# Kernel optimization log

Hardware: AMD Instinct MI355X
Metric: run time of the kernel (lower is better)

## Reference

```python
import jax, jax.numpy as jnp
import numpy as np

B, S, D = 4, 2048, 1024
H, DK, DV = 16, 64, 64


def setup_inputs() -> dict:
    key = jax.random.key(0)
    ks = jax.random.split(key, 12)
    sd = 1.0 / np.sqrt(D)
    sdo = 1.0 / np.sqrt(DV * H)
    return {
        "query": jax.random.normal(ks[0], (B, S, D), jnp.float32),
        "key": jax.random.normal(ks[1], (B, S, D), jnp.float32),
        "value": jax.random.normal(ks[2], (B, S, D), jnp.float32),
        "mask": jnp.zeros((B, 1, 1, S), jnp.float32),
        "Wq": jax.random.uniform(ks[3], (D, DK * H), jnp.float32, -sd, sd),
        "bq": jax.random.uniform(ks[4], (DK * H,), jnp.float32, -sd, sd),
        "Wk": jax.random.uniform(ks[5], (D, DK * H), jnp.float32, -sd, sd),
        "bk": jax.random.uniform(ks[6], (DK * H,), jnp.float32, -sd, sd),
        "Wv": jax.random.uniform(ks[7], (D, DV * H), jnp.float32, -sd, sd),
        "bv": jax.random.uniform(ks[8], (DV * H,), jnp.float32, -sd, sd),
        "Wo": jax.random.uniform(ks[9], (DV * H, D), jnp.float32, -sdo, sdo),
        "bo": jax.random.uniform(ks[10], (D,), jnp.float32, -sdo, sdo),
    }


def reference(query, key, value, mask, Wq, bq, Wk, bk, Wv, bv, Wo, bo):
    b, sq, _ = query.shape
    # QKV projections -> (B, H, S, d)
    Q = (query @ Wq + bq).reshape(b, sq, H, DK).transpose(0, 2, 1, 3)
    K = (key @ Wk + bk).reshape(b, key.shape[1], H, DK).transpose(0, 2, 1, 3)
    V = (value @ Wv + bv).reshape(b, value.shape[1], H, DV).transpose(0, 2, 1, 3)
    # scaled dot-product attention with additive mask
    scores = jnp.einsum("bhqd,bhkd->bhqk", Q, K) / jnp.sqrt(jnp.float32(DK))
    scores = scores + mask  # mask broadcast over heads/query positions
    probs = jax.nn.softmax(scores, axis=-1)
    # weighted values, merge heads -> (B, S, H*DV)
    weights = jnp.einsum("bhqk,bhkd->bhqd", probs, V).transpose(0, 2, 1, 3).reshape(b, sq, H * DV)
    output = weights @ Wo + bo  # dropout p=0 (eval) -> identity
    return (output, weights)
```

## Files before the change

kernel.cpp:

```cpp
#include <hip/hip_runtime.h>
#include <hip/hip_bf16.h>

typedef __attribute__((ext_vector_type(8))) short bf16x8;
typedef __attribute__((ext_vector_type(8))) short short8v;
typedef __attribute__((ext_vector_type(4))) float f32x4;

__device__ __forceinline__ short f2bf(float x) {
  union { __hip_bfloat16 h; short s; } u;
  u.h = __float2bfloat16(x);
  return u.s;
}

__device__ __forceinline__ void async16(const void* g, void* l) {
  __builtin_amdgcn_global_load_lds(
      (const __attribute__((address_space(1))) unsigned int*)g,
      (__attribute__((address_space(3))) unsigned int*)l, 16, 0, 0);
}

#define VM_WAIT4 do { asm volatile("s_waitcnt vmcnt(4)" ::: "memory"); \
                      __builtin_amdgcn_sched_barrier(0); } while (0)
#define VM_WAIT0 do { asm volatile("s_waitcnt vmcnt(0)" ::: "memory"); \
                      __builtin_amdgcn_sched_barrier(0); } while (0)

__device__ __forceinline__ void stage8k(const char* gbase, int rowStride, short* lds, int tid) {
  int wave = tid >> 6, lane = tid & 63;
#pragma unroll
  for (int j = 0; j < 2; ++j) {
    int chunk = wave * 128 + j * 64 + lane;
    int row = chunk >> 3;
    int colb = (chunk & 7) << 4;
    const char* src = gbase + row * rowStride + (colb ^ ((row & 7) << 4));
    char* dst = (char*)lds + (wave * 128 + j * 64) * 16;
    async16(src, dst);
  }
}

__global__ __launch_bounds__(256) void cvtw_k(const float* Wq, const float* Wk,
                                              const float* Wv, const float* Wo, short* Wt) {
  __shared__ short T[64 * 72];
  int mat = blockIdx.z;
  const float* src = mat == 0 ? Wq : (mat == 1 ? Wk : (mat == 2 ? Wv : Wo));
  int n0 = blockIdx.x * 64, k0 = blockIdx.y * 64;
  int tid = threadIdx.x;
#pragma unroll
  for (int i = 0; i < 4; ++i) {
    int f = i * 256 + tid;
    int kk = f >> 4, nn4 = (f & 15) * 4;
    float4 v = *(const float4*)(src + (size_t)(k0 + kk) * 1024 + n0 + nn4);
    short* d = &T[kk * 72 + nn4];
    d[0] = f2bf(v.x); d[1] = f2bf(v.y); d[2] = f2bf(v.z); d[3] = f2bf(v.w);
  }
  __syncthreads();
  short* dstm = Wt + (size_t)mat * 1048576;
#pragma unroll
  for (int i = 0; i < 2; ++i) {
    int cidx = i * 256 + tid;
    int nn = cidx >> 3, kc = (cidx & 7) * 8;
    short8v o;
#pragma unroll
    for (int j = 0; j < 8; ++j) o[j] = T[(kc + j) * 72 + nn];
    *(short8v*)(dstm + (size_t)(n0 + nn) * 1024 + k0 + kc) = o;
  }
}

__global__ __launch_bounds__(256) void cvta_k(const float* q, const float* k,
                                              const float* v, short* out) {
  int z = blockIdx.y;
  const float* src = z == 0 ? q : (z == 1 ? k : v);
  size_t base = ((size_t)blockIdx.x * 256 + threadIdx.x) * 8;
  float4 a = *(const float4*)(src + base);
  float4 b2 = *(const float4*)(src + base + 4);
  short8v h;
  h[0] = f2bf(a.x);  h[1] = f2bf(a.y);  h[2] = f2bf(a.z);  h[3] = f2bf(a.w);
  h[4] = f2bf(b2.x); h[5] = f2bf(b2.y); h[6] = f2bf(b2.z); h[7] = f2bf(b2.w);
  *(short8v*)(out + (size_t)z * 8388608 + base) = h;
}

template <int MODE>
__global__ __launch_bounds__(256) void gemm_k(
    const short* Ab, const short* Wt, const float* bias0, const float* bias1,
    short* Qp, short* Kp, short* Vpt, float* outF) {
  __shared__ short As[2][128 * 32];
  __shared__ short Bs[2][128 * 32];
  int tid = threadIdx.x, lane = tid & 63, wave = tid >> 6;
  int g = lane >> 4, c = lane & 15;
  int orig = blockIdx.x + blockIdx.y * 8;
  int wg = (orig & 7) * 64 + (orig >> 3);
  int n0 = (wg & 7) * 128, m0 = (wg >> 3) * 128, z = blockIdx.z;

  const short* Az = (MODE == 0) ? Ab + (size_t)z * 8388608 : Ab;
  const short* Wz = (MODE == 0) ? Wt + (size_t)z * 1048576 : Wt;
  const float* bias = (MODE == 0) ? (z == 0 ? bias0 : bias1) : bias0;

  auto stage = [&](int ks, int buf) {
    const char* ga = (const char*)Az + ((size_t)m0 * 1024 + ks * 32) * 2;
    const char* gb = (const char*)Wz + ((size_t)n0 * 1024 + ks * 32) * 2;
#pragma unroll
    for (int i = 0; i < 2; ++i) {
      int ch = i * 256 + tid;
      int row = ch >> 2, slot = ch & 3;
      int sw = ((row >> 1) & 3) << 4;
      char* dstA = (char*)&As[buf][0] + (i * 256 + wave * 64) * 16;
      char* dstB = (char*)&Bs[buf][0] + (i * 256 + wave * 64) * 16;
      async16(ga + (size_t)row * 2048 + ((slot << 4) ^ sw), dstA);
      async16(gb + (size_t)row * 2048 + ((slot << 4) ^ sw), dstB);
    }
  };

  f32x4 acc[4][4];
#pragma unroll
  for (int i = 0; i < 4; ++i)
#pragma unroll
    for (int j = 0; j < 4; ++j) acc[i][j] = (f32x4){0.f, 0.f, 0.f, 0.f};

  int wr = (wave >> 1) * 64, wc = (wave & 1) * 64;

  stage(0, 0);
  for (int ks = 0; ks < 32; ++ks) {
    if (ks + 1 < 32) { stage(ks + 1, (ks & 1) ^ 1); VM_WAIT4; }
    else             { VM_WAIT0; }
    __builtin_amdgcn_s_barrier();
    int cur = ks & 1;
    bf16x8 af[4], bfv[4];
#pragma unroll
    for (int mt = 0; mt < 4; ++mt) {
      int r_ = wr + mt * 16 + c;
      af[mt] = *(const bf16x8*)((const char*)&As[cur][0] + r_ * 64 +
                                ((g << 4) ^ ((((r_ >> 1) & 3)) << 4)));
    }
#pragma unroll
    for (int nt = 0; nt < 4; ++nt) {
      int r_ = wc + nt * 16 + c;
      bfv[nt] = *(const bf16x8*)((const char*)&Bs[cur][0] + r_ * 64 +
                                 ((g << 4) ^ ((((r_ >> 1) & 3)) << 4)));
    }
    __builtin_amdgcn_s_setprio(1);
#pragma unroll
    for (int mt = 0; mt < 4; ++mt)
#pragma unroll
      for (int nt = 0; nt < 4; ++nt) {
        if (MODE == 1)
          acc[mt][nt] = __builtin_amdgcn_mfma_f32_16x16x32_bf16(af[mt], bfv[nt], acc[mt][nt], 0, 0, 0);
        else
          acc[mt][nt] = __builtin_amdgcn_mfma_f32_16x16x32_bf16(bfv[nt], af[mt], acc[mt][nt], 0, 0, 0);
      }
    __builtin_amdgcn_s_setprio(0);
    __builtin_amdgcn_s_barrier();
  }

  if (MODE == 0) {
    short* dst0 = (z == 0) ? Qp : Kp;
    float scale = (z == 0) ? 0.125f : 1.f;
#pragma unroll
    for (int nt = 0; nt < 4; ++nt) {
      int nb = n0 + wc + nt * 16 + g * 4;
      float4 b4 = *(const float4*)(bias + nb);
      int d0 = nb & 63, nh = nb >> 6;
#pragma unroll
      for (int mt = 0; mt < 4; ++mt) {
        int m = m0 + wr + mt * 16 + c;
        int bh = (m >> 11) * 16 + nh;
        short4 hv;
        hv.x = f2bf((acc[mt][nt][0] + b4.x) * scale);
        hv.y = f2bf((acc[mt][nt][1] + b4.y) * scale);
        hv.z = f2bf((acc[mt][nt][2] + b4.z) * scale);
        hv.w = f2bf((acc[mt][nt][3] + b4.w) * scale);
        *(short4*)(dst0 + ((size_t)bh * 2048 + (m & 2047)) * 64 + d0) = hv;
      }
    }
  } else if (MODE == 1) {
#pragma unroll
    for (int nt = 0; nt < 4; ++nt) {
      int n = n0 + wc + nt * 16 + c;
      float bb = bias[n];
      int d = n & 63, nh = n >> 6;
#pragma unroll
      for (int mt = 0; mt < 4; ++mt) {
        int mb = m0 + wr + mt * 16 + g * 4;
        int bh = (mb >> 11) * 16 + nh;
        short4 hv;
        hv.x = f2bf(acc[mt][nt][0] + bb);
        hv.y = f2bf(acc[mt][nt][1] + bb);
        hv.z = f2bf(acc[mt][nt][2] + bb);
        hv.w = f2bf(acc[mt][nt][3] + bb);
        *(short4*)(Vpt + ((size_t)bh * 64 + d) * 2048 + (mb & 2047)) = hv;
      }
    }
  } else {
#pragma unroll
    for (int nt = 0; nt < 4; ++nt) {
      int nb = n0 + wc + nt * 16 + g * 4;
      float4 b4 = *(const float4*)(bias + nb);
#pragma unroll
      for (int mt = 0; mt < 4; ++mt) {
        int m = m0 + wr + mt * 16 + c;
        float4 o;
        o.x = acc[mt][nt][0] + b4.x;
        o.y = acc[mt][nt][1] + b4.y;
        o.z = acc[mt][nt][2] + b4.z;
        o.w = acc[mt][nt][3] + b4.w;
        *(float4*)(outF + (size_t)m * 1024 + nb) = o;
      }
    }
  }
}

__global__ __launch_bounds__(256) void attn_k(const short* Qp, const short* Kp,
                                              const short* Vpt, const float* mask,
                                              float* outW, short* wbf) {
  __shared__ short Qs[64 * 64];
  __shared__ short Ks[2][64 * 64];
  __shared__ short Vs[2][64 * 64];
  short* Ps = Qs;
  int tid = threadIdx.x, lane = tid & 63, wave = tid >> 6;
  int g = lane >> 4, c = lane & 15;
  int orig = blockIdx.x + blockIdx.y * 32;
  int wg = (orig & 7) * 256 + (orig >> 3);
  int qt = wg & 31, bh = wg >> 5;
  int b = bh >> 4, h = bh & 15;

  const char* Qg = (const char*)Qp + ((size_t)bh * 2048 + qt * 64) * 128;
  const char* Kg = (const char*)Kp + (size_t)bh * 2048 * 128;
  const char* Vg = (const char*)Vpt + (size_t)bh * 64 * 4096;

  stage8k(Qg, 128, Qs, tid);
  stage8k(Kg, 128, Ks[0], tid);
  stage8k(Vg, 4096, Vs[0], tid);

  f32x4 acco[4];
#pragma unroll
  for (int i = 0; i < 4; ++i) acco[i] = (f32x4){0.f, 0.f, 0.f, 0.f};
  float mrun = -1e30f, lrun = 0.f;

  VM_WAIT4;
  int qrow = wave * 16 + c;
  bf16x8 aq[2];
#pragma unroll
  for (int k2 = 0; k2 < 2; ++k2)
    aq[k2] = *(const bf16x8*)((const char*)Qs + qrow * 128 +
                              ((k2 * 64 + g * 16) ^ ((qrow & 7) << 4)));

  int cur = 0;
  for (int t = 0; t < 32; ++t) {
    float4 mk[4];
#pragma unroll
    for (int n = 0; n < 4; ++n)
      mk[n] = *(const float4*)(mask + (size_t)b * 2048 + t * 64 + n * 16 + g * 4);
    __builtin_amdgcn_sched_barrier(0);
    if (t + 1 < 32) {
      stage8k(Kg + (size_t)(t + 1) * 8192, 128, Ks[cur ^ 1], tid);
      stage8k(Vg + (size_t)(t + 1) * 128, 4096, Vs[cur ^ 1], tid);
    }
    VM_WAIT4;
    __builtin_amdgcn_s_barrier();
    f32x4 sc[4];
    __builtin_amdgcn_s_setprio(1);
#pragma unroll
    for (int n = 0; n < 4; ++n) {
      sc[n] = (f32x4){0.f, 0.f, 0.f, 0.f};
#pragma unroll
      for (int k2 = 0; k2 < 2; ++k2) {
        int row = n * 16 + c;
        bf16x8 bk = *(const bf16x8*)((const char*)&Ks[cur][0] + row * 128 +
                                     ((k2 * 64 + g * 16) ^ ((row & 7) << 4)));
        sc[n] = __builtin_amdgcn_mfma_f32_16x16x32_bf16(bk, aq[k2], sc[n], 0, 0, 0);
      }
    }
    __builtin_amdgcn_s_setprio(0);
#pragma unroll
    for (int n = 0; n < 4; ++n) {
      sc[n][0] += mk[n].x; sc[n][1] += mk[n].y;
      sc[n][2] += mk[n].z; sc[n][3] += mk[n].w;
    }
    float tmax = sc[0][0];
#pragma unroll
    for (int n = 0; n < 4; ++n)
#pragma unroll
      for (int r = 0; r < 4; ++r) tmax = fmaxf(tmax, sc[n][r]);
    tmax = fmaxf(tmax, __shfl_xor(tmax, 16));
    tmax = fmaxf(tmax, __shfl_xor(tmax, 32));
    if (!__all(tmax <= mrun + 8.0f)) {
      float mnew = fmaxf(mrun, tmax);
      float fsc = __expf(mrun - mnew);
      mrun = mnew;
      lrun *= fsc;
#pragma unroll
      for (int n = 0; n < 4; ++n)
#pragma unroll
        for (int r = 0; r < 4; ++r) acco[n][r] *= fsc;
    }
    float p[4][4], rs = 0.f;
#pragma unroll
    for (int n = 0; n < 4; ++n)
#pragma unroll
      for (int r = 0; r < 4; ++r) {
        p[n][r] = __expf(sc[n][r] - mrun);
        rs += p[n][r];
      }
    rs += __shfl_xor(rs, 16);
    rs += __shfl_xor(rs, 32);
    lrun += rs;
#pragma unroll
    for (int n = 0; n < 4; ++n) {
      short4 hv;
      hv.x = f2bf(p[n][0]); hv.y = f2bf(p[n][1]);
      hv.z = f2bf(p[n][2]); hv.w = f2bf(p[n][3]);
      int colb = (n * 32 + g * 8) ^ ((qrow & 7) << 4);
      *(short4*)((char*)Ps + qrow * 128 + colb) = hv;
    }
    __builtin_amdgcn_s_setprio(1);
#pragma unroll
    for (int k2 = 0; k2 < 2; ++k2) {
      bf16x8 ap = *(const bf16x8*)((const char*)Ps + qrow * 128 +
                                   ((k2 * 64 + g * 16) ^ ((qrow & 7) << 4)));
#pragma unroll
      for (int n2 = 0; n2 < 4; ++n2) {
        int rv = n2 * 16 + c;
        bf16x8 bv = *(const bf16x8*)((const char*)&Vs[cur][0] + rv * 128 +
                                     ((k2 * 64 + g * 16) ^ ((rv & 7) << 4)));
        acco[n2] = __builtin_amdgcn_mfma_f32_16x16x32_bf16(bv, ap, acco[n2], 0, 0, 0);
      }
    }
    __builtin_amdgcn_s_setprio(0);
    __builtin_amdgcn_s_barrier();
    cur ^= 1;
  }
  float inv = 1.0f / lrun;
  int srow = qt * 64 + qrow;
#pragma unroll
  for (int n = 0; n < 4; ++n) {
    int col0 = h * 64 + n * 16 + g * 4;
    size_t idx = ((size_t)b * 2048 + srow) * 1024 + col0;
    float4 o;
    o.x = acco[n][0] * inv; o.y = acco[n][1] * inv;
    o.z = acco[n][2] * inv; o.w = acco[n][3] * inv;
    *(float4*)(outW + idx) = o;
    short4 hv;
    hv.x = f2bf(o.x); hv.y = f2bf(o.y); hv.z = f2bf(o.z); hv.w = f2bf(o.w);
    *(short4*)(wbf + idx) = hv;
  }
}

extern "C" void kernel_launch(void* const* d_in, const int* in_sizes, int n_in,
                              void* d_out, int out_size, void* d_ws, size_t ws_size,
                              hipStream_t stream) {
  const float* q    = (const float*)d_in[0];
  const float* k    = (const float*)d_in[1];
  const float* v    = (const float*)d_in[2];
  const float* mask = (const float*)d_in[3];
  const float* Wq   = (const float*)d_in[4];
  const float* bq   = (const float*)d_in[5];
  const float* Wk   = (const float*)d_in[6];
  const float* bk   = (const float*)d_in[7];
  const float* Wv   = (const float*)d_in[8];
  const float* bv   = (const float*)d_in[9];
  const float* Wo   = (const float*)d_in[10];
  const float* bo   = (const float*)d_in[11];

  short* Wt  = (short*)d_ws;
  short* Qp  = Wt + (size_t)4 * 1048576;
  short* Kp  = Qp + (size_t)8388608;
  short* Vpt = Kp + (size_t)8388608;
  short* Wbf = Vpt + (size_t)8388608;

  float* out1 = (float*)d_out;
  float* out2 = out1 + (size_t)8388608;

  short* Abf = (short*)d_out;

  cvtw_k<<<dim3(16, 16, 4), dim3(256), 0, stream>>>(Wq, Wk, Wv, Wo, Wt);
  cvta_k<<<dim3(4096, 3), dim3(256), 0, stream>>>(q, k, v, Abf);
  gemm_k<0><<<dim3(8, 64, 2), dim3(256), 0, stream>>>(
      Abf, Wt, bq, bk, Qp, Kp, (short*)nullptr, (float*)nullptr);
  gemm_k<1><<<dim3(8, 64, 1), dim3(256), 0, stream>>>(
      Abf + (size_t)2 * 8388608, Wt + (size_t)2 * 1048576, bv, (const float*)nullptr,
      (short*)nullptr, (short*)nullptr, Vpt, (float*)nullptr);
  attn_k<<<dim3(32, 64), dim3(256), 0, stream>>>(Qp, Kp, Vpt, mask, out2, Wbf);
  gemm_k<2><<<dim3(8, 64, 1), dim3(256), 0, stream>>>(
      Wbf, Wt + (size_t)3 * 1048576, bo, (const float*)nullptr,
      (short*)nullptr, (short*)nullptr, (short*)nullptr, out1);
}
```

Measured before the change: 426.1 us.

## Fuse Q/K/V projections into one GEMM launch, narrow output-GEMM tiles, vectorize softmax

Merges the separate QK and V projection launches into a single GEMM grid over 3072 output columns, choosing the Q/K/V segment from the column index. The V segment now writes its transposed layout with scalar bf16 stores. The output projection uses 128x64 tiles, doubling the block count to improve occupancy across CUs. The attention softmax is rewritten with 2-wide float vectors to encourage packed FP32 ops. The aim is to cut launch overhead and tail effects, at the cost of uncoalesced scalar stores for V.

Result: faster. 396.5 us (-6.9%).

```diff
diff --git a/kernel.cpp b/kernel.cpp
--- a/kernel.cpp
+++ b/kernel.cpp
@@ -4,6 +4,7 @@
 typedef __attribute__((ext_vector_type(8))) short bf16x8;
 typedef __attribute__((ext_vector_type(8))) short short8v;
 typedef __attribute__((ext_vector_type(4))) float f32x4;
+typedef __attribute__((ext_vector_type(2))) float f32x2;
 
 __device__ __forceinline__ short f2bf(float x) {
   union { __hip_bfloat16 h; short s; } u;
@@ -18,6 +19,8 @@
 }
 
 #define VM_WAIT4 do { asm volatile("s_waitcnt vmcnt(4)" ::: "memory"); \
+                      __builtin_amdgcn_sched_barrier(0); } while (0)
+#define VM_WAIT3 do { asm volatile("s_waitcnt vmcnt(3)" ::: "memory"); \
                       __builtin_amdgcn_sched_barrier(0); } while (0)
 #define VM_WAIT0 do { asm volatile("s_waitcnt vmcnt(0)" ::: "memory"); \
                       __builtin_amdgcn_sched_barrier(0); } while (0)
@@ -78,19 +81,28 @@
 
 template <int MODE>
 __global__ __launch_bounds__(256) void gemm_k(
-    const short* Ab, const short* Wt, const float* bias0, const float* bias1,
-    short* Qp, short* Kp, short* Vpt, float* outF) {
+    const short* Ab, const short* Wt, const float* b0, const float* b1,
+    const float* b2, short* Qp, short* Kp, short* Vpt, float* outF) {
+  constexpr int BN = (MODE == 0) ? 128 : 64;
+  constexpr int NT = BN / 32;
   __shared__ short As[2][128 * 32];
-  __shared__ short Bs[2][128 * 32];
+  __shared__ short Bs[2][BN * 32];
   int tid = threadIdx.x, lane = tid & 63, wave = tid >> 6;
   int g = lane >> 4, c = lane & 15;
-  int orig = blockIdx.x + blockIdx.y * 8;
-  int wg = (orig & 7) * 64 + (orig >> 3);
-  int n0 = (wg & 7) * 128, m0 = (wg >> 3) * 128, z = blockIdx.z;
-
-  const short* Az = (MODE == 0) ? Ab + (size_t)z * 8388608 : Ab;
-  const short* Wz = (MODE == 0) ? Wt + (size_t)z * 1048576 : Wt;
-  const float* bias = (MODE == 0) ? (z == 0 ? bias0 : bias1) : bias0;
+  int n0, m0;
+  if (MODE == 0) {
+    int orig = blockIdx.x + blockIdx.y * 24;
+    int wg = (orig & 7) * 192 + (orig >> 3);
+    n0 = (wg % 24) * 128; m0 = (wg / 24) * 128;
+  } else {
+    int orig = blockIdx.x + blockIdx.y * 16;
+    int wg = (orig & 7) * 128 + (orig >> 3);
+    n0 = (wg & 15) * 64; m0 = (wg >> 4) * 128;
+  }
+  int seg = n0 >> 10;
+  const short* Az = (MODE == 0) ? Ab + (size_t)seg * 8388608 : Ab;
+  const short* Wz = Wt;
+  const float* bias = (MODE == 0) ? (seg == 0 ? b0 : (seg == 1 ? b1 : b2)) : b0;
 
   auto stage = [&](int ks, int buf) {
     const char* ga = (const char*)Az + ((size_t)m0 * 1024 + ks * 32) * 2;
@@ -101,27 +113,37 @@
       int row = ch >> 2, slot = ch & 3;
       int sw = ((row >> 1) & 3) << 4;
       char* dstA = (char*)&As[buf][0] + (i * 256 + wave * 64) * 16;
+      async16(ga + (size_t)row * 2048 + ((slot << 4) ^ sw), dstA);
+    }
+#pragma unroll
+    for (int i = 0; i < BN / 64; ++i) {
+      int ch = i * 256 + tid;
+      int row = ch >> 2, slot = ch & 3;
+      int sw = ((row >> 1) & 3) << 4;
       char* dstB = (char*)&Bs[buf][0] + (i * 256 + wave * 64) * 16;
-      async16(ga + (size_t)row * 2048 + ((slot << 4) ^ sw), dstA);
       async16(gb + (size_t)row * 2048 + ((slot << 4) ^ sw), dstB);
     }
   };
 
-  f32x4 acc[4][4];
+  f32x4 acc[4][NT];
 #pragma unroll
   for (int i = 0; i < 4; ++i)
 #pragma unroll
-    for (int j = 0; j < 4; ++j) acc[i][j] = (f32x4){0.f, 0.f, 0.f, 0.f};
-
-  int wr = (wave >> 1) * 64, wc = (wave & 1) * 64;
+    for (int j = 0; j < NT; ++j) acc[i][j] = (f32x4){0.f, 0.f, 0.f, 0.f};
+
+  int wr = (wave >> 1) * 64, wc = (wave & 1) * (BN / 2);
 
   stage(0, 0);
   for (int ks = 0; ks < 32; ++ks) {
-    if (ks + 1 < 32) { stage(ks + 1, (ks & 1) ^ 1); VM_WAIT4; }
-    else             { VM_WAIT0; }
+    if (ks + 1 < 32) {
+      stage(ks + 1, (ks & 1) ^ 1);
+      if (MODE == 0) { VM_WAIT4; } else { VM_WAIT3; }
+    } else {
+      VM_WAIT0;
+    }
     __builtin_amdgcn_s_barrier();
     int cur = ks & 1;
-    bf16x8 af[4], bfv[4];
+    bf16x8 af[4], bfv[NT];
 #pragma unroll
     for (int mt = 0; mt < 4; ++mt) {
       int r_ = wr + mt * 16 + c;
@@ -129,7 +151,7 @@
                                 ((g << 4) ^ ((((r_ >> 1) & 3)) << 4)));
     }
 #pragma unroll
-    for (int nt = 0; nt < 4; ++nt) {
+    for (int nt = 0; nt < NT; ++nt) {
       int r_ = wc + nt * 16 + c;
       bfv[nt] = *(const bf16x8*)((const char*)&Bs[cur][0] + r_ * 64 +
                                  ((g << 4) ^ ((((r_ >> 1) & 3)) << 4)));
@@ -138,57 +160,47 @@
 #pragma unroll
     for (int mt = 0; mt < 4; ++mt)
 #pragma unroll
-      for (int nt = 0; nt < 4; ++nt) {
-        if (MODE == 1)
-          acc[mt][nt] = __builtin_amdgcn_mfma_f32_16x16x32_bf16(af[mt], bfv[nt], acc[mt][nt], 0, 0, 0);
-        else
-          acc[mt][nt] = __builtin_amdgcn_mfma_f32_16x16x32_bf16(bfv[nt], af[mt], acc[mt][nt], 0, 0, 0);
-      }
+      for (int nt = 0; nt < NT; ++nt)
+        acc[mt][nt] = __builtin_amdgcn_mfma_f32_16x16x32_bf16(bfv[nt], af[mt], acc[mt][nt], 0, 0, 0);
     __builtin_amdgcn_s_setprio(0);
     __builtin_amdgcn_s_barrier();
   }
 
   if (MODE == 0) {
-    short* dst0 = (z == 0) ? Qp : Kp;
-    float scale = (z == 0) ? 0.125f : 1.f;
-#pragma unroll
-    for (int nt = 0; nt < 4; ++nt) {
+    float scale = (seg == 0) ? 0.125f : 1.f;
+#pragma unroll
+    for (int nt = 0; nt < NT; ++nt) {
       int nb = n0 + wc + nt * 16 + g * 4;
-      float4 b4 = *(const float4*)(bias + nb);
-      int d0 = nb & 63, nh = nb >> 6;
-#pragma unroll
-      for (int mt = 0; mt < 4; ++mt) {
-        int m = m0 + wr + mt * 16 + c;
-        int bh = (m >> 11) * 16 + nh;
-        short4 hv;
-        hv.x = f2bf((acc[mt][nt][0] + b4.x) * scale);
-        hv.y = f2bf((acc[mt][nt][1] + b4.y) * scale);
-        hv.z = f2bf((acc[mt][nt][2] + b4.z) * scale);
-        hv.w = f2bf((acc[mt][nt][3] + b4.w) * scale);
-        *(short4*)(dst0 + ((size_t)bh * 2048 + (m & 2047)) * 64 + d0) = hv;
+      float4 b4 = *(const float4*)(bias + (nb & 1023));
+      float bb[4] = {b4.x, b4.y, b4.z, b4.w};
+      int d0 = nb & 63, nh = (nb >> 6) & 15;
+      if (seg < 2) {
+        short* dst0 = (seg == 0) ? Qp : Kp;
+#pragma unroll
+        for (int mt = 0; mt < 4; ++mt) {
+          int m = m0 + wr + mt * 16 + c;
+          int bh = (m >> 11) * 16 + nh;
+          short4 hv;
+          hv.x = f2bf((acc[mt][nt][0] + bb[0]) * scale);
+          hv.y = f2bf((acc[mt][nt][1] + bb[1]) * scale);
+          hv.z = f2bf((acc[mt][nt][2] + bb[2]) * scale);
+          hv.w = f2bf((acc[mt][nt][3] + bb[3]) * scale);
+          *(short4*)(dst0 + ((size_t)bh * 2048 + (m & 2047)) * 64 + d0) = hv;
+        }
+      } else {
+#pragma unroll
+        for (int mt = 0; mt < 4; ++mt) {
+          int m = m0 + wr + mt * 16 + c;
+          int s = m & 2047, bh = (m >> 11) * 16 + nh;
+#pragma unroll
+          for (int r = 0; r < 4; ++r)
+            Vpt[((size_t)bh * 64 + d0 + r) * 2048 + s] = f2bf(acc[mt][nt][r] + bb[r]);
+        }
       }
     }
-  } else if (MODE == 1) {
-#pragma unroll
-    for (int nt = 0; nt < 4; ++nt) {
-      int n = n0 + wc + nt * 16 + c;
-      float bb = bias[n];
-      int d = n & 63, nh = n >> 6;
-#pragma unroll
-      for (int mt = 0; mt < 4; ++mt) {
-        int mb = m0 + wr + mt * 16 + g * 4;
-        int bh = (mb >> 11) * 16 + nh;
-        short4 hv;
-        hv.x = f2bf(acc[mt][nt][0] + bb);
-        hv.y = f2bf(acc[mt][nt][1] + bb);
-        hv.z = f2bf(acc[mt][nt][2] + bb);
-        hv.w = f2bf(acc[mt][nt][3] + bb);
-        *(short4*)(Vpt + ((size_t)bh * 64 + d) * 2048 + (mb & 2047)) = hv;
-      }
-    }
   } else {
 #pragma unroll
-    for (int nt = 0; nt < 4; ++nt) {
+    for (int nt = 0; nt < NT; ++nt) {
       int nb = n0 + wc + nt * 16 + g * 4;
       float4 b4 = *(const float4*)(bias + nb);
 #pragma unroll
@@ -267,16 +279,16 @@
       }
     }
     __builtin_amdgcn_s_setprio(0);
+    f32x2 sv[8];
 #pragma unroll
     for (int n = 0; n < 4; ++n) {
-      sc[n][0] += mk[n].x; sc[n][1] += mk[n].y;
-      sc[n][2] += mk[n].z; sc[n][3] += mk[n].w;
-    }
-    float tmax = sc[0][0];
-#pragma unroll
-    for (int n = 0; n < 4; ++n)
-#pragma unroll
-      for (int r = 0; r < 4; ++r) tmax = fmaxf(tmax, sc[n][r]);
+      f32x2 mlo = {mk[n].x, mk[n].y}, mhi = {mk[n].z, mk[n].w};
+      sv[2 * n]     = __builtin_shufflevector(sc[n], sc[n], 0, 1) + mlo;
+      sv[2 * n + 1] = __builtin_shufflevector(sc[n], sc[n], 2, 3) + mhi;
+    }
+    float tmax = fmaxf(sv[0][0], sv[0][1]);
+#pragma unroll
+    for (int i = 1; i < 8; ++i) tmax = fmaxf(tmax, fmaxf(sv[i][0], sv[i][1]));
     tmax = fmaxf(tmax, __shfl_xor(tmax, 16));
     tmax = fmaxf(tmax, __shfl_xor(tmax, 32));
     if (!__all(tmax <= mrun + 8.0f)) {
@@ -285,26 +297,27 @@
       mrun = mnew;
       lrun *= fsc;
 #pragma unroll
-      for (int n = 0; n < 4; ++n)
-#pragma unroll
-        for (int r = 0; r < 4; ++r) acco[n][r] *= fsc;
-    }
-    float p[4][4], rs = 0.f;
-#pragma unroll
-    for (int n = 0; n < 4; ++n)
-#pragma unroll
-      for (int r = 0; r < 4; ++r) {
-        p[n][r] = __expf(sc[n][r] - mrun);
-        rs += p[n][r];
-      }
+      for (int n = 0; n < 4; ++n) acco[n] *= fsc;
+    }
+    f32x2 mr2 = {mrun, mrun};
+    f32x2 rs2 = {0.f, 0.f};
+    f32x2 p2[8];
+#pragma unroll
+    for (int i = 0; i < 8; ++i) {
+      f32x2 e = sv[i] - mr2;
+      f32x2 pe = {__expf(e[0]), __expf(e[1])};
+      p2[i] = pe;
+      rs2 += pe;
+    }
+    float rs = rs2[0] + rs2[1];
     rs += __shfl_xor(rs, 16);
     rs += __shfl_xor(rs, 32);
     lrun += rs;
 #pragma unroll
     for (int n = 0; n < 4; ++n) {
       short4 hv;
-      hv.x = f2bf(p[n][0]); hv.y = f2bf(p[n][1]);
-      hv.z = f2bf(p[n][2]); hv.w = f2bf(p[n][3]);
+      hv.x = f2bf(p2[2 * n][0]);     hv.y = f2bf(p2[2 * n][1]);
+      hv.z = f2bf(p2[2 * n + 1][0]); hv.w = f2bf(p2[2 * n + 1][1]);
       int colb = (n * 32 + g * 8) ^ ((qrow & 7) << 4);
       *(short4*)((char*)Ps + qrow * 128 + colb) = hv;
     }
@@ -331,9 +344,8 @@
   for (int n = 0; n < 4; ++n) {
     int col0 = h * 64 + n * 16 + g * 4;
     size_t idx = ((size_t)b * 2048 + srow) * 1024 + col0;
-    float4 o;
-    o.x = acco[n][0] * inv; o.y = acco[n][1] * inv;
-    o.z = acco[n][2] * inv; o.w = acco[n][3] * inv;
+    f32x4 o4 = acco[n] * inv;
+    float4 o = {o4[0], o4[1], o4[2], o4[3]};
     *(float4*)(outW + idx) = o;
     short4 hv;
     hv.x = f2bf(o.x); hv.y = f2bf(o.y); hv.z = f2bf(o.z); hv.w = f2bf(o.w);
@@ -370,13 +382,10 @@
 
   cvtw_k<<<dim3(16, 16, 4), dim3(256), 0, stream>>>(Wq, Wk, Wv, Wo, Wt);
   cvta_k<<<dim3(4096, 3), dim3(256), 0, stream>>>(q, k, v, Abf);
-  gemm_k<0><<<dim3(8, 64, 2), dim3(256), 0, stream>>>(
-      Abf, Wt, bq, bk, Qp, Kp, (short*)nullptr, (float*)nullptr);
-  gemm_k<1><<<dim3(8, 64, 1), dim3(256), 0, stream>>>(
-      Abf + (size_t)2 * 8388608, Wt + (size_t)2 * 1048576, bv, (const float*)nullptr,
-      (short*)nullptr, (short*)nullptr, Vpt, (float*)nullptr);
+  gemm_k<0><<<dim3(24, 64), dim3(256), 0, stream>>>(
+      Abf, Wt, bq, bk, bv, Qp, Kp, Vpt, (float*)nullptr);
   attn_k<<<dim3(32, 64), dim3(256), 0, stream>>>(Qp, Kp, Vpt, mask, out2, Wbf);
-  gemm_k<2><<<dim3(8, 64, 1), dim3(256), 0, stream>>>(
-      Wbf, Wt + (size_t)3 * 1048576, bo, (const float*)nullptr,
+  gemm_k<2><<<dim3(16, 64), dim3(256), 0, stream>>>(
+      Wbf, Wt + (size_t)3 * 1048576, bo, (const float*)nullptr, (const float*)nullptr,
       (short*)nullptr, (short*)nullptr, (short*)nullptr, out1);
 }
```
